# Optimization experiments

Hardware: AMD Instinct MI355X
Metric: run time of the kernel (lower is better)

## Reference

```python
import jax, jax.numpy as jnp
import numpy as np

N_GRAPHS = 1024   # pool of learnable adjacency blocks (len(Adjs))
BLOCK = 128       # nodes per graph (block size)
BATCH = 1024      # len(batch_idrange); D = BATCH * BLOCK rows
FEAT = 32         # input feature dim


def setup_inputs() -> dict:
    key = jax.random.key(0)
    k1, k2, k3 = jax.random.split(key, 3)
    # learnable per-graph adjacency weights (self.weights stacked)
    weights = jax.random.normal(k1, (N_GRAPHS, BLOCK, BLOCK), dtype=jnp.float32)
    # dense node-feature input [D, F] with D = BATCH * BLOCK
    inp = jax.random.normal(k2, (BATCH * BLOCK, FEAT), dtype=jnp.float32)
    # which adjacency block each batch element uses
    batch_idrange = jax.random.randint(k3, (BATCH,), 0, N_GRAPHS, dtype=jnp.int64)
    return {"input": inp, "weights": weights, "batch_idrange": batch_idrange}


def reference(input, weights, batch_idrange):
    # Original: blockdiag(weights[batch_idrange]) @ input.
    # Block-diagonal structure means each block only touches its own row slab,
    # so this is exactly a batched per-block matmul (same math, no zero padding).
    B = batch_idrange.shape[0]
    n = weights.shape[1]
    W = weights[batch_idrange]                    # [B, n, n] gather (irregular access)
    xb = input.reshape(B, n, -1)                  # [B, n, F]
    out = jnp.einsum('bij,bjf->bif', W, xb)       # [B, n, F]
    return out.reshape(input.shape[0], -1)        # [D, F]
```

## Files before the change

kernel.cpp:

```cpp
#include <hip/hip_runtime.h>

#define NODES 128
#define FEAT  32
#define XPAD  136

typedef __attribute__((ext_vector_type(8))) short bf16x8;
typedef __attribute__((ext_vector_type(4))) float f32x4;

__device__ __forceinline__ unsigned pk_bf16(float a, float b) {
    unsigned ua = __builtin_bit_cast(unsigned, a);
    unsigned ub = __builtin_bit_cast(unsigned, b);
    ua += 0x7fffu + ((ua >> 16) & 1u);
    ub += 0x7fffu + ((ub >> 16) & 1u);
    return (ua >> 16) | (ub & 0xffff0000u);
}

__device__ __forceinline__ bf16x8 cvt_frag(float4 lo, float4 hi) {
    union { unsigned u[4]; bf16x8 v; } r;
    r.u[0] = pk_bf16(lo.x, lo.y);
    r.u[1] = pk_bf16(lo.z, lo.w);
    r.u[2] = pk_bf16(hi.x, hi.y);
    r.u[3] = pk_bf16(hi.z, hi.w);
    return r.v;
}

__global__ __launch_bounds__(512, 8)
void blockdiag_mm(const float* __restrict__ inp,
                  const float* __restrict__ weights,
                  const int* __restrict__ idx,
                  float* __restrict__ out)
{
    __shared__ __align__(16) short xt[FEAT * XPAD];

    const int b  = blockIdx.x;
    const int u  = threadIdx.x;
    const int w  = u >> 6;
    const int l  = u & 63;
    const int ln = l & 15;
    const int q  = l >> 4;

    const float* __restrict__ xin = inp + (size_t)b * (NODES * FEAT);
    const float* __restrict__ wb  = weights + (size_t)idx[b] * (NODES * NODES);

    float4 a[4][2];
    {
        const float* ar = wb + (16 * w + ln) * NODES + q * 8;
        #pragma unroll
        for (int kc = 0; kc < 4; ++kc) {
            a[kc][0] = *(const float4*)(ar + kc * 32);
            a[kc][1] = *(const float4*)(ar + kc * 32 + 4);
        }
    }

    {
        const float4* x4 = (const float4*)xin;
        const int fq = u & 7;
        const int k0 = (u >> 3) * 2;
        float4 v0 = x4[k0 * 8 + fq];
        float4 v1 = x4[(k0 + 1) * 8 + fq];
        const float pv0[4] = {v0.x, v0.y, v0.z, v0.w};
        const float pv1[4] = {v1.x, v1.y, v1.z, v1.w};
        #pragma unroll
        for (int i = 0; i < 4; ++i)
            *(unsigned*)(&xt[(fq * 4 + i) * XPAD + k0]) = pk_bf16(pv0[i], pv1[i]);
    }
    __syncthreads();

    f32x4 acc[2] = {};

    #pragma unroll
    for (int kc = 0; kc < 4; ++kc) {
        const bf16x8 afr = cvt_frag(a[kc][0], a[kc][1]);
        #pragma unroll
        for (int nt = 0; nt < 2; ++nt) {
            const bf16x8 bfr = *(const bf16x8*)(&xt[(16 * nt + ln) * XPAD + kc * 32 + q * 8]);
            acc[nt] = __builtin_amdgcn_mfma_f32_16x16x32_bf16(afr, bfr, acc[nt], 0, 0, 0);
        }
    }

    float* ob = out + (size_t)b * (NODES * FEAT);
    #pragma unroll
    for (int nt = 0; nt < 2; ++nt)
        #pragma unroll
        for (int reg = 0; reg < 4; ++reg)
            ob[(16 * w + q * 4 + reg) * FEAT + 16 * nt + ln] = acc[nt][reg];
}

extern "C" void kernel_launch(void* const* d_in, const int* in_sizes, int n_in,
                              void* d_out, int out_size, void* d_ws, size_t ws_size,
                              hipStream_t stream) {
    const float* inp = (const float*)d_in[0];
    const float* wts = (const float*)d_in[1];
    const int*   idx = (const int*)d_in[2];
    float* outp = (float*)d_out;
    const int B = in_sizes[2];
    hipLaunchKernelGGL(blockdiag_mm, dim3(B), dim3(512), 0, stream,
                       inp, wts, idx, outp);
}
```

Baseline: 110.3 us.

## Stage weight tiles through LDS via direct global-to-LDS loads in two phases

Weight rows are no longer loaded into registers. They are copied straight into shared memory with global_load_lds in two 64-column halves, using a rotated (swizzled) segment layout to avoid bank conflicts. A-fragments are then read from LDS and converted to bf16. This is meant to use wider, more coalesced DMA-style loads and lower register pressure, at the cost of 32KB of extra LDS, extra barriers between the halves, and lower occupancy (launch bounds drop from 8 to 6).

Measured after the change: 108.6 us. Within noise of the previous version (-1.5%).

```diff
diff --git a/kernel.cpp b/kernel.cpp
--- a/kernel.cpp
+++ b/kernel.cpp
@@ -6,6 +6,9 @@
 
 typedef __attribute__((ext_vector_type(8))) short bf16x8;
 typedef __attribute__((ext_vector_type(4))) float f32x4;
+
+typedef const __attribute__((address_space(1))) void gvoid;
+typedef __attribute__((address_space(3))) void       svoid;
 
 __device__ __forceinline__ unsigned pk_bf16(float a, float b) {
     unsigned ua = __builtin_bit_cast(unsigned, a);
@@ -24,13 +27,14 @@
     return r.v;
 }
 
-__global__ __launch_bounds__(512, 8)
+__global__ __launch_bounds__(512, 6)
 void blockdiag_mm(const float* __restrict__ inp,
                   const float* __restrict__ weights,
                   const int* __restrict__ idx,
                   float* __restrict__ out)
 {
-    __shared__ __align__(16) short xt[FEAT * XPAD];
+    __shared__ __align__(16) float4 wc[NODES * 16];
+    __shared__ __align__(16) short  xt[FEAT * XPAD];
 
     const int b  = blockIdx.x;
     const int u  = threadIdx.x;
@@ -42,22 +46,28 @@
     const float* __restrict__ xin = inp + (size_t)b * (NODES * FEAT);
     const float* __restrict__ wb  = weights + (size_t)idx[b] * (NODES * NODES);
 
-    float4 a[4][2];
-    {
-        const float* ar = wb + (16 * w + ln) * NODES + q * 8;
+    const float4* x4 = (const float4*)xin;
+    const int fq = u & 7;
+    const int k0 = (u >> 3) * 2;
+    const float4 v0 = x4[k0 * 8 + fq];
+    const float4 v1 = x4[(k0 + 1) * 8 + fq];
+
+    auto stage_w = [&](int p) {
         #pragma unroll
-        for (int kc = 0; kc < 4; ++kc) {
-            a[kc][0] = *(const float4*)(ar + kc * 32);
-            a[kc][1] = *(const float4*)(ar + kc * 32 + 4);
+        for (int s = 0; s < 4; ++s) {
+            const int i    = s * 512 + u;
+            const int row  = i >> 4;
+            const int lseg = i & 15;
+            const int gseg = (lseg - row) & 15;
+            gvoid* g   = (gvoid*)(wb + row * NODES + p * 64 + gseg * 4);
+            svoid* dst = (svoid*)(wc + s * 512 + w * 64);
+            __builtin_amdgcn_global_load_lds(g, dst, 16, 0, 0);
         }
-    }
+    };
+
+    stage_w(0);
 
     {
-        const float4* x4 = (const float4*)xin;
-        const int fq = u & 7;
-        const int k0 = (u >> 3) * 2;
-        float4 v0 = x4[k0 * 8 + fq];
-        float4 v1 = x4[(k0 + 1) * 8 + fq];
         const float pv0[4] = {v0.x, v0.y, v0.z, v0.w};
         const float pv1[4] = {v1.x, v1.y, v1.z, v1.w};
         #pragma unroll
@@ -67,14 +77,27 @@
     __syncthreads();
 
     f32x4 acc[2] = {};
+    const int arow = 16 * w + ln;
 
     #pragma unroll
-    for (int kc = 0; kc < 4; ++kc) {
-        const bf16x8 afr = cvt_frag(a[kc][0], a[kc][1]);
+    for (int p = 0; p < 2; ++p) {
+        if (p == 1) {
+            __syncthreads();
+            stage_w(1);
+            __syncthreads();
+        }
         #pragma unroll
-        for (int nt = 0; nt < 2; ++nt) {
-            const bf16x8 bfr = *(const bf16x8*)(&xt[(16 * nt + ln) * XPAD + kc * 32 + q * 8]);
-            acc[nt] = __builtin_amdgcn_mfma_f32_16x16x32_bf16(afr, bfr, acc[nt], 0, 0, 0);
+        for (int kcp = 0; kcp < 2; ++kcp) {
+            const int kb = 2 * p + kcp;
+            const int g0 = kcp * 8 + q * 2;
+            const float4 alo = wc[arow * 16 + ((g0 + 0 + arow) & 15)];
+            const float4 ahi = wc[arow * 16 + ((g0 + 1 + arow) & 15)];
+            const bf16x8 afr = cvt_frag(alo, ahi);
+            #pragma unroll
+            for (int nt = 0; nt < 2; ++nt) {
+                const bf16x8 bfr = *(const bf16x8*)(&xt[(16 * nt + ln) * XPAD + kb * 32 + q * 8]);
+                acc[nt] = __builtin_amdgcn_mfma_f32_16x16x32_bf16(afr, bfr, acc[nt], 0, 0, 0);
+            }
         }
     }
 
```
